# Performance work log

Hardware: AMD Instinct MI355X
Metric: run time of the kernel (lower is better)

Reference implementation:

```python
import jax, jax.numpy as jnp
import numpy as np

# Kobayashi dendrite-growth parameters (init_params values from the repo)
TAU = 3e-4
EPSILONB = 0.01
KAPPA = 1.8
DELTA = 0.02
ANISO = 6.0
ALPHA = 0.9
GAMMA = 10.0
TEQ = 1.0
THETA0 = 0.2
PIX = 4.0 * np.arctan(1.0)  # pi
DX = 0.03
DY = 0.03
DT = 1e-4

B, H, W = 4, 2048, 2048


def lap(u, dx, dy):
    # 5-point Laplacian, periodic boundaries. x = last axis, y = second-to-last.
    return ((jnp.roll(u, -1, -1) + jnp.roll(u, 1, -1) - 2.0 * u) / (dx * dx)
            + (jnp.roll(u, -1, -2) + jnp.roll(u, 1, -2) - 2.0 * u) / (dy * dy))


def grad(u, axis_name, d):
    ax = -1 if axis_name == 'x' else -2
    return (jnp.roll(u, -1, ax) - jnp.roll(u, 1, ax)) / (2.0 * d)


def setup_inputs() -> dict:
    key = jax.random.key(0)
    k1, k2 = jax.random.split(key)
    phi = jax.random.uniform(k1, (B, H, W), dtype=jnp.float32)
    tempr = jax.random.uniform(k2, (B, H, W), dtype=jnp.float32)
    return {"phi": phi, "tempr": tempr}


def reference(phi, tempr):
    lap_phi = lap(phi, DX, DY)
    lap_tempr = lap(tempr, DX, DY)
    phidx = grad(phi, 'x', DX)
    phidy = grad(phi, 'y', DY)
    theta = jnp.arctan2(phidy, phidx)
    epsilon = EPSILONB * (1.0 + DELTA * jnp.cos(ANISO * (theta - THETA0)))
    epsilon_deriv = -EPSILONB * ANISO * DELTA * jnp.sin(ANISO * (theta - THETA0))
    prod_mat1 = epsilon * epsilon_deriv * phidx
    prod_mat2 = -epsilon * epsilon_deriv * phidy
    term1 = grad(prod_mat1, 'y', DY)
    term2 = grad(prod_mat2, 'x', DX)
    m = ALPHA / PIX * jnp.arctan(GAMMA * (TEQ - tempr))
    dphi_dt = DT / TAU * (term1 + term2 + epsilon ** 2 * lap_phi
                          + phi * (1.0 - phi) * (phi - 0.5 + m))
    phi_new = phi + dphi_dt
    tempr_new = tempr + DT * lap_tempr + KAPPA * dphi_dt
    return (phi_new, tempr_new)
```

## Files before the change

kernel.cpp:

```cpp
#include <hip/hip_runtime.h>
#include <math.h>


#define Bz 4
#define Hd 2048
#define Wd 2048
#define TX 64
#define TY 32
#define PW (TX + 4)
#define PH (TY + 4)
#define QW (TX + 2)
#define QH (TY + 2)

#define INV2D   16.6666666666667f
#define INVD2   1111.11111111111f
#define DT_TAU  0.333333333333333f
#define DTc     1e-4f
#define KAPPAc  1.8f
#define EPSB    0.01f
#define DELTAc  0.02f
#define ANISOc  6.0f
#define A_PI    0.2864788975654116f
#define GAMMAc  10.0f
#define TEQc    1.0f
#define C6T0    0.3623577544766736f
#define S6T0    0.9320390859672263f

__global__ __launch_bounds__(256) void dendrite_step(
    const float* __restrict__ phi, const float* __restrict__ tempr,
    float* __restrict__ out_phi, float* __restrict__ out_tempr)
{
    __shared__ float sphi[PH * PW];
    __shared__ float sp1[QH * QW];
    __shared__ float sp2[QH * QW];
    __shared__ float se2[QH * QW];

    const int tid = threadIdx.x;
    const int x0 = blockIdx.x * TX;
    const int y0 = blockIdx.y * TY;
    const int base = blockIdx.z * (Hd * Wd);

    for (int i = tid; i < PH * PW; i += 256) {
        int r = i / PW;
        int c = i - r * PW;
        int gy = (y0 + r - 2) & (Hd - 1);
        int gx = (x0 + c - 2) & (Wd - 1);
        sphi[i] = phi[base + gy * Wd + gx];
    }
    __syncthreads();

    for (int i = tid; i < QH * QW; i += 256) {
        int r = i / QW;
        int c = i - r * QW;
        int p = (r + 1) * PW + (c + 1);
        float phidx = (sphi[p + 1]  - sphi[p - 1])  * INV2D;
        float phidy = (sphi[p + PW] - sphi[p - PW]) * INV2D;

        float r2 = phidx * phidx + phidy * phidy;
        float rinv = (r2 > 0.0f) ? rsqrtf(r2) : 0.0f;
        float ct = (r2 > 0.0f) ? phidx * rinv : 1.0f;
        float st = phidy * rinv;

        float c2 = ct * ct - st * st;
        float s2 = 2.0f * ct * st;
        float c4 = c2 * c2 - s2 * s2;
        float s4 = 2.0f * c2 * s2;
        float c6 = c4 * c2 - s4 * s2;
        float s6 = s4 * c2 + c4 * s2;

        float cosA = c6 * C6T0 + s6 * S6T0;
        float sinA = s6 * C6T0 - c6 * S6T0;

        float eps  = EPSB * (1.0f + DELTAc * cosA);
        float epsd = -EPSB * ANISOc * DELTAc * sinA;
        float ee   = eps * epsd;

        sp1[i] = ee * phidx;
        sp2[i] = -ee * phidy;
        se2[i] = eps * eps;
    }
    __syncthreads();

    const int tx = tid & 63;
    const int ty0 = tid >> 6;

    for (int k = 0; k < TY / 4; ++k) {
        int y = ty0 + k * 4;
        int q = (y + 1) * QW + (tx + 1);
        int p = (y + 2) * PW + (tx + 2);

        float term1 = (sp1[q + QW] - sp1[q - QW]) * INV2D;
        float term2 = (sp2[q + 1]  - sp2[q - 1])  * INV2D;

        float phic = sphi[p];
        float lap_phi = (sphi[p + 1] + sphi[p - 1] - 2.0f * phic) * INVD2
                      + (sphi[p + PW] + sphi[p - PW] - 2.0f * phic) * INVD2;

        int gy = y0 + y;
        int gx = x0 + tx;
        int gxp = (gx + 1) & (Wd - 1);
        int gxm = (gx - 1) & (Wd - 1);
        int gyp = (gy + 1) & (Hd - 1);
        int gym = (gy - 1) & (Hd - 1);
        int rowb = base + gy * Wd;

        float tc = tempr[rowb + gx];
        float lap_t = (tempr[rowb + gxp] + tempr[rowb + gxm] - 2.0f * tc) * INVD2
                    + (tempr[base + gyp * Wd + gx] + tempr[base + gym * Wd + gx]
                       - 2.0f * tc) * INVD2;

        float m = A_PI * atanf(GAMMAc * (TEQc - tc));
        float dphi = DT_TAU * (term1 + term2 + se2[q] * lap_phi
                               + phic * (1.0f - phic) * (phic - 0.5f + m));

        int gidx = rowb + gx;
        out_phi[gidx] = phic + dphi;
        out_tempr[gidx] = tc + DTc * lap_t + KAPPAc * dphi;
    }
}

extern "C" void kernel_launch(void* const* d_in, const int* in_sizes, int n_in,
                              void* d_out, int out_size, void* d_ws, size_t ws_size,
                              hipStream_t stream) {
    const float* phi = (const float*)d_in[0];
    const float* tempr = (const float*)d_in[1];
    float* out_phi = (float*)d_out;
    float* out_tempr = out_phi + (size_t)Bz * Hd * Wd;

    dim3 grid(Wd / TX, Hd / TY, Bz);
    dendrite_step<<<grid, 256, 0, stream>>>(phi, tempr, out_phi, out_tempr);
}
```

Before: 285.9 us.

## Rewrite stencil as register-streaming wavefront with lane permutes and fast atan

Replaces the shared-memory tiled kernel with a per-wavefront column strip that marches down rows, keeping a rolling window of phi/tempr values in registers. Horizontal neighbours come from ds_bpermute instead of LDS, which removes the barriers and the halo recomputation. The anisotropy terms are recomputed via double-angle identities with a reciprocal instead of rsqrt, and atanf is replaced by a minimax polynomial. The strip overlaps by two lanes per wave and the polynomial atan may reduce accuracy.

```diff
diff --git a/kernel.cpp b/kernel.cpp
--- a/kernel.cpp
+++ b/kernel.cpp
@@ -5,15 +5,12 @@
 #define Bz 4
 #define Hd 2048
 #define Wd 2048
-#define TX 64
-#define TY 32
-#define PW (TX + 4)
-#define PH (TY + 4)
-#define QW (TX + 2)
-#define QH (TY + 2)
+#define STRIP 62
+#define RB    32
+#define NSX   34
 
-#define INV2D   16.6666666666667f
 #define INVD2   1111.11111111111f
+#define K1      277.777777777778f
 #define DT_TAU  0.333333333333333f
 #define DTc     1e-4f
 #define KAPPAc  1.8f
@@ -25,98 +22,118 @@
 #define TEQc    1.0f
 #define C6T0    0.3623577544766736f
 #define S6T0    0.9320390859672263f
+#define PI_2    1.5707963267948966f
 
-__global__ __launch_bounds__(256) void dendrite_step(
+__device__ __forceinline__ float perm(int addr, float v) {
+    return __int_as_float(__builtin_amdgcn_ds_bpermute(addr, __float_as_int(v)));
+}
+
+__device__ __forceinline__ void prodc(float dx, float dy,
+                                      float& p1, float& p2, float& e2)
+{
+    float dx2 = dx * dx;
+    float r2  = fmaf(dy, dy, dx2);
+    float cn  = fmaf(-dy, dy, dx2);
+    float irr = __builtin_amdgcn_rcpf(fmaxf(r2, 1e-20f));
+    float c2  = cn * irr;
+    float s2  = 2.0f * dx * dy * irr;
+    float c22 = c2 * c2;
+    float s22 = s2 * s2;
+    float c6  = c2 * fmaf(4.0f, c22, -3.0f);
+    float s6  = s2 * fmaf(-4.0f, s22, 3.0f);
+    float cosA = fmaf(c6, C6T0, s6 * S6T0);
+    float sinA = fmaf(s6, C6T0, -c6 * S6T0);
+    float eps  = fmaf(EPSB * DELTAc, cosA, EPSB);
+    float ee   = eps * (-EPSB * ANISOc * DELTAc) * sinA;
+    p1 = ee * dx;
+    p2 = -ee * dy;
+    e2 = eps * eps;
+}
+
+__device__ __forceinline__ float atan_fast(float g) {
+    float r  = __builtin_amdgcn_rcpf(g);
+    float a  = fminf(g, r);
+    float a2 = a * a;
+    float p  = a * fmaf(a2, fmaf(a2, 0.079331f, -0.288679f), 0.995354f);
+    return (g <= 1.0f) ? p : PI_2 - p;
+}
+
+__global__ __launch_bounds__(256, 6) void dendrite_step(
     const float* __restrict__ phi, const float* __restrict__ tempr,
     float* __restrict__ out_phi, float* __restrict__ out_tempr)
 {
-    __shared__ float sphi[PH * PW];
-    __shared__ float sp1[QH * QW];
-    __shared__ float sp2[QH * QW];
-    __shared__ float se2[QH * QW];
+    const int lane = threadIdx.x & 63;
+    const int wid  = threadIdx.x >> 6;
+    const int bx   = blockIdx.x;
+    const int ybase = blockIdx.y * (RB * 4) + wid * RB;
+    const size_t base = (size_t)blockIdx.z * (size_t)(Hd * Wd);
 
-    const int tid = threadIdx.x;
-    const int x0 = blockIdx.x * TX;
-    const int y0 = blockIdx.y * TY;
-    const int base = blockIdx.z * (Hd * Wd);
+    const int col  = (bx * STRIP - 1 + lane) & (Wd - 1);
+    const int scol = (bx * STRIP - 1 + lane) & (Wd - 1);
+    const bool do_store = ((unsigned)(lane - 1) < (unsigned)STRIP);
+    const int pL = ((lane - 1) & 63) * 4;
+    const int pR = ((lane + 1) & 63) * 4;
 
-    for (int i = tid; i < PH * PW; i += 256) {
-        int r = i / PW;
-        int c = i - r * PW;
-        int gy = (y0 + r - 2) & (Hd - 1);
-        int gx = (x0 + c - 2) & (Wd - 1);
-        sphi[i] = phi[base + gy * Wd + gx];
+    const float* Pp = phi + base;
+    const float* Tp = tempr + base;
+
+#define RIDX(r) ((((r) & (Hd - 1)) * Wd))
+
+    float cm1 = Pp[RIDX(ybase - 1) + col];
+    float c0  = Pp[RIDX(ybase)     + col];
+    float cp1 = Pp[RIDX(ybase + 1) + col];
+    float cp2 = Pp[RIDX(ybase + 2) + col];
+    float cm2 = Pp[RIDX(ybase - 2) + col];
+
+    float lm1 = perm(pL, cm1), rm1 = perm(pR, cm1);
+    float lY  = perm(pL, c0 ), rY  = perm(pR, c0 );
+    float lY1 = perm(pL, cp1), rY1 = perm(pR, cp1);
+    float lY2 = perm(pL, cp2), rY2 = perm(pR, cp2);
+
+    float p1m, p2m_, e2m_;
+    prodc(rm1 - lm1, c0 - cm2, p1m, p2m_, e2m_);
+    float p1c, p2c, e2c;
+    prodc(rY - lY, cp1 - cm1, p1c, p2c, e2c);
+    float p2cL = perm(pL, p2c), p2cR = perm(pR, p2c);
+
+    float tm = Tp[RIDX(ybase - 1) + col];
+    float tc = Tp[RIDX(ybase)     + col];
+    float tcL = perm(pL, tc), tcR = perm(pR, tc);
+
+    #pragma unroll 4
+    for (int k = 0; k < RB; ++k) {
+        const int y = ybase + k;
+
+        float cNew = Pp[RIDX(y + 3) + col];
+        float tNew = Tp[RIDX(y + 1) + col];
+
+        float p1p, p2p, e2p;
+        prodc(rY1 - lY1, cp2 - c0, p1p, p2p, e2p);
+        float p2pL = perm(pL, p2p), p2pR = perm(pR, p2p);
+
+        float term12  = (p1p - p1m + p2cR - p2cL) * K1;
+        float lap_phi = (lY + rY + cm1 + cp1 - 4.0f * c0) * INVD2;
+        float lap_t   = (tcL + tcR + tm + tNew - 4.0f * tc) * INVD2;
+        float mm   = A_PI * atan_fast(GAMMAc * (TEQc - tc));
+        float dphi = DT_TAU * (term12 + e2c * lap_phi
+                               + c0 * (1.0f - c0) * (c0 - 0.5f + mm));
+
+        if (do_store) {
+            size_t gi = base + (size_t)y * Wd + scol;
+            out_phi[gi]   = c0 + dphi;
+            out_tempr[gi] = fmaf(KAPPAc, dphi, fmaf(DTc, lap_t, tc));
+        }
+
+        cm1 = c0; c0 = cp1; cp1 = cp2; cp2 = cNew;
+        lY = lY1; rY = rY1; lY1 = lY2; rY1 = rY2;
+        lY2 = perm(pL, cNew); rY2 = perm(pR, cNew);
+        p1m = p1c; p1c = p1p;
+        p2cL = p2pL; p2cR = p2pR;
+        e2c = e2p;
+        tm = tc; tc = tNew;
+        tcL = perm(pL, tNew); tcR = perm(pR, tNew);
     }
-    __syncthreads();
-
-    for (int i = tid; i < QH * QW; i += 256) {
-        int r = i / QW;
-        int c = i - r * QW;
-        int p = (r + 1) * PW + (c + 1);
-        float phidx = (sphi[p + 1]  - sphi[p - 1])  * INV2D;
-        float phidy = (sphi[p + PW] - sphi[p - PW]) * INV2D;
-
-        float r2 = phidx * phidx + phidy * phidy;
-        float rinv = (r2 > 0.0f) ? rsqrtf(r2) : 0.0f;
-        float ct = (r2 > 0.0f) ? phidx * rinv : 1.0f;
-        float st = phidy * rinv;
-
-        float c2 = ct * ct - st * st;
-        float s2 = 2.0f * ct * st;
-        float c4 = c2 * c2 - s2 * s2;
-        float s4 = 2.0f * c2 * s2;
-        float c6 = c4 * c2 - s4 * s2;
-        float s6 = s4 * c2 + c4 * s2;
-
-        float cosA = c6 * C6T0 + s6 * S6T0;
-        float sinA = s6 * C6T0 - c6 * S6T0;
-
-        float eps  = EPSB * (1.0f + DELTAc * cosA);
-        float epsd = -EPSB * ANISOc * DELTAc * sinA;
-        float ee   = eps * epsd;
-
-        sp1[i] = ee * phidx;
-        sp2[i] = -ee * phidy;
-        se2[i] = eps * eps;
-    }
-    __syncthreads();
-
-    const int tx = tid & 63;
-    const int ty0 = tid >> 6;
-
-    for (int k = 0; k < TY / 4; ++k) {
-        int y = ty0 + k * 4;
-        int q = (y + 1) * QW + (tx + 1);
-        int p = (y + 2) * PW + (tx + 2);
-
-        float term1 = (sp1[q + QW] - sp1[q - QW]) * INV2D;
-        float term2 = (sp2[q + 1]  - sp2[q - 1])  * INV2D;
-
-        float phic = sphi[p];
-        float lap_phi = (sphi[p + 1] + sphi[p - 1] - 2.0f * phic) * INVD2
-                      + (sphi[p + PW] + sphi[p - PW] - 2.0f * phic) * INVD2;
-
-        int gy = y0 + y;
-        int gx = x0 + tx;
-        int gxp = (gx + 1) & (Wd - 1);
-        int gxm = (gx - 1) & (Wd - 1);
-        int gyp = (gy + 1) & (Hd - 1);
-        int gym = (gy - 1) & (Hd - 1);
-        int rowb = base + gy * Wd;
-
-        float tc = tempr[rowb + gx];
-        float lap_t = (tempr[rowb + gxp] + tempr[rowb + gxm] - 2.0f * tc) * INVD2
-                    + (tempr[base + gyp * Wd + gx] + tempr[base + gym * Wd + gx]
-                       - 2.0f * tc) * INVD2;
-
-        float m = A_PI * atanf(GAMMAc * (TEQc - tc));
-        float dphi = DT_TAU * (term1 + term2 + se2[q] * lap_phi
-                               + phic * (1.0f - phic) * (phic - 0.5f + m));
-
-        int gidx = rowb + gx;
-        out_phi[gidx] = phic + dphi;
-        out_tempr[gidx] = tc + DTc * lap_t + KAPPAc * dphi;
-    }
+#undef RIDX
 }
 
 extern "C" void kernel_launch(void* const* d_in, const int* in_sizes, int n_in,
@@ -127,6 +144,6 @@
     float* out_phi = (float*)d_out;
     float* out_tempr = out_phi + (size_t)Bz * Hd * Wd;
 
-    dim3 grid(Wd / TX, Hd / TY, Bz);
+    dim3 grid(NSX, Hd / (RB * 4), Bz);
     dendrite_step<<<grid, 256, 0, stream>>>(phi, tempr, out_phi, out_tempr);
 }
```

New measurement: 291.6 us. About the same (+2.0%).
